# Kernel tuning notes

Measured on AMD Instinct MI355X. Metric: run time of the kernel, lower is better.

## Reference

```python
import jax, jax.numpy as jnp
import numpy as np

B, H, N, D = 2, 16, 2048, 64

def setup_inputs() -> dict:
    key = jax.random.key(0)
    ks = jax.random.split(key, 5)
    q = jax.random.normal(ks[0], (B, H, N, D), dtype=jnp.float32)
    k = jax.random.normal(ks[1], (B, H, N, D), dtype=jnp.float32)
    v = jax.random.normal(ks[2], (B, H, N, D), dtype=jnp.float32)
    # 1x1 Conv2d(heads, heads, bias=False) == HxH linear mixing over the head dim
    W_pre = jax.random.normal(ks[3], (H, H), dtype=jnp.float32) * (1.0 / jnp.sqrt(H))
    W_post = jax.random.normal(ks[4], (H, H), dtype=jnp.float32) * (1.0 / jnp.sqrt(H))
    return {"q": q, "k": k, "v": v, "W_pre": W_pre, "W_post": W_post}

def reference(q, k, v, W_pre, W_post):
    heads = q.shape[1]
    d_head = q.shape[-1]
    # original: scale = (1/sqrt(heads)) / sqrt(d_head)
    scale = 1.0 / (jnp.sqrt(jnp.float32(heads)) * jnp.sqrt(jnp.float32(d_head)))
    # pre-softmax talking heads applied to BOTH q and k (head-mixing linear)
    q = jnp.einsum('ef,bfnd->bend', W_pre, q)
    k = jnp.einsum('ef,bfnd->bend', W_pre, k)
    attn_weights = jnp.einsum('bhid,bhjd->bhij', q, k) * scale  # [B,H,N,N]
    i = q.shape[-2]
    j = k.shape[-2]
    causal_mask = jnp.triu(jnp.ones((i, j), dtype=bool), k=1)
    attn_weights = jnp.where(causal_mask, -jnp.inf, attn_weights)
    # softmax computed in float32 (dtype=torch.float32 in attn_fn)
    attn_probs = jax.nn.softmax(attn_weights.astype(jnp.float32), axis=-1)
    # dropout p=0.0 -> identity
    attn_probs = jnp.einsum('ef,bfij->beij', W_post, attn_probs)
    attn_output = jnp.einsum('bhij,bhjd->bhid', attn_probs, v)
    return attn_output
```

## Files before the change

### kernel.cpp

```cpp
#include <hip/hip_runtime.h>
#include <math.h>

typedef _Float16 Hh;
typedef __attribute__((ext_vector_type(8))) _Float16 half8;
typedef __attribute__((ext_vector_type(4))) _Float16 half4;
typedef __attribute__((ext_vector_type(4))) float float4v;

#define B_ 2
#define H_ 16
#define N_ 2048
#define D_ 64
#define ND_ (N_*D_)
#define C1 0.04508422f

#define BAR() asm volatile("s_waitcnt lgkmcnt(0)\n\ts_barrier" ::: "memory")

#define EB_JS 644
#define EB_IS 20
#define PM_ES 1280
#define PM_IS 40

__global__ __launch_bounds__(256,2) void prep_kernel(const float* __restrict__ q,
    const float* __restrict__ k, const float* __restrict__ v,
    const float* __restrict__ Wpre,
    Hh* __restrict__ qb, Hh* __restrict__ kb, Hh* __restrict__ vt2,
    float4* __restrict__ out4, float4* __restrict__ lacc4)
{
    int tid = threadIdx.x;
    int bid = blockIdx.x;
    if (bid < 512) {
        __shared__ float wsh[256];
        wsh[tid] = Wpre[tid];
        __syncthreads();
        int tensor = bid >> 8;
        int g = ((bid & 255) << 8) | tid;
        int b = g >> 15;
        int r = g & 32767;
        const float4* src = (const float4*)(tensor ? k : q);
        Hh* dst = tensor ? kb : qb;
        float4 x[16];
        #pragma unroll
        for (int f=0; f<16; f++) x[f] = src[(size_t)(b*16+f)*32768 + r];
        #pragma unroll
        for (int e=0; e<16; e++) {
            float4 a = make_float4(0.f,0.f,0.f,0.f);
            #pragma unroll
            for (int f=0; f<16; f++) {
                float wv = wsh[e*16+f];
                a.x += wv*x[f].x; a.y += wv*x[f].y; a.z += wv*x[f].z; a.w += wv*x[f].w;
            }
            half4 hv; hv[0]=(Hh)a.x; hv[1]=(Hh)a.y; hv[2]=(Hh)a.z; hv[3]=(Hh)a.w;
            *(half4*)(dst + (size_t)(b*16+e)*ND_ + (size_t)r*4) = hv;
        }
    } else if (bid < 768) {
        __shared__ Hh tile[64*48];
        int tb = bid - 512;
        int be = tb >> 3;
        int jtg = tb & 7;
        const float4* v4 = (const float4*)v;
        for (int u=0; u<8; u++) {
            int jt = jtg*8 + u;
            #pragma unroll
            for (int p=0; p<2; p++) {
                int j = p*16 + (tid>>4);
                int d4 = tid & 15;
                float4 val = v4[(size_t)be*32768 + (size_t)(jt*32+j)*16 + d4];
                tile[(d4*4+0)*48 + j] = (Hh)val.x;
                tile[(d4*4+1)*48 + j] = (Hh)val.y;
                tile[(d4*4+2)*48 + j] = (Hh)val.z;
                tile[(d4*4+3)*48 + j] = (Hh)val.w;
            }
            BAR();
            {
                int d = tid >> 2;
                int jc = (tid & 3) * 8;
                half8 o;
                #pragma unroll
                for (int z=0; z<8; z++) o[z] = tile[d*48 + jc + z];
                *(half8*)(vt2 + ((size_t)(be*64) + jt)*2048 + (size_t)tid*8) = o;
            }
            BAR();
        }
    } else {
        int zid = (bid - 768) * 256 + tid;
        float4 zz = make_float4(0.f,0.f,0.f,0.f);
        #pragma unroll
        for (int u=0; u<4; u++) out4[(size_t)u*262144 + zid] = zz;
        if (zid < 16384) lacc4[zid] = zz;
    }
}

__global__ __launch_bounds__(1024,4) void denom_kernel(const Hh* __restrict__ qb,
    const Hh* __restrict__ kb, float* __restrict__ lacc_g)
{
    int bid = blockIdx.x;
    int s = bid & 7;
    int idx = bid >> 3;
    int b = idx & 1;
    int pr = idx >> 1;
    int tid = threadIdx.x;
    int lane = tid & 63, w = tid >> 6;
    int qd = lane >> 4, c = lane & 15;

    const Hh* qh = qb + (size_t)(b*16 + w)*ND_;
    const Hh* kh = kb + (size_t)(b*16 + w)*ND_;

    for (int hf = 0; hf < 2; hf++) {
        int it = hf ? (63 - pr) : pr;
        if (s > it) continue;
        int i0 = it * 32;

        half8 aq[2][2];
        #pragma unroll
        for (int ig=0; ig<2; ig++) {
            const Hh* qr = qh + (size_t)(i0 + ig*16 + c)*64 + qd*8;
            aq[ig][0] = *(const half8*)qr;
            aq[ig][1] = *(const half8*)(qr+32);
        }
        float lacc[2][4];
        #pragma unroll
        for (int ig=0; ig<2; ig++)
            #pragma unroll
            for (int r=0; r<4; r++) lacc[ig][r] = 0.f;

        for (int jt = s; jt <= it; jt += 8) {
            int j0 = jt*32;
            #pragma unroll
            for (int jh=0; jh<2; jh++) {
                const Hh* kr = kh + (size_t)(j0 + jh*16 + c)*64 + qd*8;
                half8 b0 = *(const half8*)kr;
                half8 b1 = *(const half8*)(kr+32);
                int j = j0 + jh*16 + c;
                #pragma unroll
                for (int ig=0; ig<2; ig++) {
                    float4v sv = {0.f,0.f,0.f,0.f};
                    sv = __builtin_amdgcn_mfma_f32_16x16x32_f16(aq[ig][0], b0, sv, 0,0,0);
                    sv = __builtin_amdgcn_mfma_f32_16x16x32_f16(aq[ig][1], b1, sv, 0,0,0);
                    #pragma unroll
                    for (int r=0; r<4; r++) {
                        int i = i0 + ig*16 + qd*4 + r;
                        float ev = (j <= i) ? __builtin_amdgcn_exp2f(sv[r]*C1) : 0.f;
                        lacc[ig][r] += ev;
                    }
                }
            }
        }
        #pragma unroll
        for (int ig=0; ig<2; ig++) {
            #pragma unroll
            for (int r=0; r<4; r++) {
                float vs = lacc[ig][r];
                vs += __shfl_xor(vs, 1);
                vs += __shfl_xor(vs, 2);
                vs += __shfl_xor(vs, 4);
                vs += __shfl_xor(vs, 8);
                if (c == 0)
                    unsafeAtomicAdd(&lacc_g[(size_t)(b*16+w)*N_ + i0 + ig*16 + qd*4 + r], vs);
            }
        }
    }
}

__global__ __launch_bounds__(1024,4) void attend_kernel(const Hh* __restrict__ qb,
    const Hh* __restrict__ kb, const Hh* __restrict__ vt2,
    const float* __restrict__ lacc_g, const float* __restrict__ Wpost,
    float* __restrict__ out)
{
    __shared__ Hh Ebuf[32*EB_JS];
    __shared__ Hh Pm[16*PM_ES];

    int bid = blockIdx.x;
    int s = (bid & 7) >> 1;
    int b = bid & 1;
    int pr = bid >> 3;

    int tid = threadIdx.x;
    int lane = tid & 63, w = tid >> 6;
    int qd = lane >> 4, c = lane & 15;

    int jh2 = w & 1, ib = 4*(w >> 1);
    half4 wf;
    #pragma unroll
    for (int z=0; z<4; z++) wf[z] = (Hh)Wpost[c*16 + qd*4 + z];

    for (int hf = 0; hf < 2; hf++) {
        int it = hf ? (63 - pr) : pr;
        if (s > it) continue;
        int i0 = it * 32;

        half8 aq[2][2];
        float lgr[2][4];
        #pragma unroll
        for (int ig=0; ig<2; ig++) {
            const Hh* qr = qb + (size_t)((b*16+w)*N_ + i0 + ig*16 + c)*64 + qd*8;
            aq[ig][0] = *(const half8*)qr;
            aq[ig][1] = *(const half8*)(qr+32);
            #pragma unroll
            for (int r=0; r<4; r++)
                lgr[ig][r] = __builtin_amdgcn_logf(
                    lacc_g[(size_t)(b*16+w)*N_ + i0 + ig*16 + qd*4 + r]);
        }

        float4v acc[2][4];
        #pragma unroll
        for (int ig=0; ig<2; ig++) for (int nc=0; nc<4; nc++)
            acc[ig][nc] = (float4v){0.f,0.f,0.f,0.f};

        auto scores = [&](int jt) {
            #pragma unroll
            for (int jh=0; jh<2; jh++) {
                int jc = jt*32 + jh*16;
                const Hh* kr = kb + (size_t)((b*16+w)*N_ + jc + c)*64 + qd*8;
                half8 b0 = *(const half8*)kr;
                half8 b1 = *(const half8*)(kr+32);
                int j = jc + c;
                #pragma unroll
                for (int ig=0; ig<2; ig++) {
                    float4v sv = {0.f,0.f,0.f,0.f};
                    sv = __builtin_amdgcn_mfma_f32_16x16x32_f16(aq[ig][0], b0, sv, 0,0,0);
                    sv = __builtin_amdgcn_mfma_f32_16x16x32_f16(aq[ig][1], b1, sv, 0,0,0);
                    #pragma unroll
                    for (int r=0; r<4; r++) {
                        int i = i0 + ig*16 + qd*4 + r;
                        float ev = (j <= i) ?
                            __builtin_amdgcn_exp2f(sv[r]*C1 - lgr[ig][r]) : 0.f;
                        Ebuf[(size_t)(jh*16+c)*EB_JS + (ig*16+qd*4+r)*EB_IS + w] = (Hh)ev;
                    }
                }
            }
        };

        scores(s);
        BAR();

        for (int jt = s; jt <= it; jt += 4) {
            #pragma unroll
            for (int ii=0; ii<4; ii++) {
                int i = ib + ii;
                half4 ef = *(const half4*)&Ebuf[(jh2*16+c)*EB_JS + i*EB_IS + qd*4];
                float4v cc = {0.f,0.f,0.f,0.f};
                cc = __builtin_amdgcn_mfma_f32_16x16x16f16(ef, wf, cc, 0,0,0);
                half4 hv;
                #pragma unroll
                for (int r=0; r<4; r++) hv[r] = (Hh)cc[r];
                *(half4*)&Pm[c*PM_ES + i*PM_IS + jh2*16 + qd*4] = hv;
            }
            BAR();
            #pragma unroll
            for (int nc=0; nc<4; nc++) {
                const Hh* vr = vt2 + (size_t)((b*16+w)*64 + jt)*2048 + (nc*16+c)*32 + qd*8;
                half8 vb = *(const half8*)vr;
                #pragma unroll
                for (int ig=0; ig<2; ig++) {
                    half8 pa = *(const half8*)&Pm[w*PM_ES + (ig*16+c)*PM_IS + qd*8];
                    acc[ig][nc] = __builtin_amdgcn_mfma_f32_16x16x32_f16(pa, vb, acc[ig][nc], 0,0,0);
                }
            }
            if (jt + 4 <= it) scores(jt + 4);
            BAR();
        }

        #pragma unroll
        for (int ig=0; ig<2; ig++) {
            #pragma unroll
            for (int nc0=0; nc0<4; nc0++) {
                int nc = (nc0 + s) & 3;
                #pragma unroll
                for (int r=0; r<4; r++)
                    unsafeAtomicAdd(&out[(size_t)((b*16+w)*N_ + i0 + ig*16 + qd*4 + r)*64 + nc*16 + c],
                                    acc[ig][nc][r]);
            }
        }
    }
}

extern "C" void kernel_launch(void* const* d_in, const int* in_sizes, int n_in,
                              void* d_out, int out_size, void* d_ws, size_t ws_size,
                              hipStream_t stream) {
    const float* q     = (const float*)d_in[0];
    const float* k     = (const float*)d_in[1];
    const float* v     = (const float*)d_in[2];
    const float* Wpre  = (const float*)d_in[3];
    const float* Wpost = (const float*)d_in[4];
    float* out = (float*)d_out;

    size_t tsz = (size_t)B_*H_*N_*D_;
    Hh* qb = (Hh*)d_ws;
    Hh* kb = qb + tsz;
    Hh* vt2 = kb + tsz;
    float* lacc = (float*)(vt2 + tsz);

    prep_kernel<<<1792, 256, 0, stream>>>(q, k, v, Wpre, qb, kb, vt2,
                                          (float4*)out, (float4*)lacc);
    denom_kernel<<<512, 1024, 0, stream>>>(qb, kb, lacc);
    attend_kernel<<<256, 1024, 0, stream>>>(qb, kb, vt2, lacc, Wpost, out);
}
```

Before: 253.7 us.

## Halve attend block to 512 threads with multi-head per-wave work and K/V prefetch

The attend kernel now runs 8 waves per block instead of 16. Each wave computes scores for 4 heads over one 16-column half and accumulates PV for 2 output heads, and it writes score tiles as half4 vectors. K and V loads are issued ahead of use: the next K tile is prefetched during the W_post mixing step, and V is loaded before the barrier. The denom kernel also gets a register double-buffered K prefetch, and the Pm shared-memory padding is shrunk. The trade-off is many more live registers per wave (4 heads of Q, K and logs, plus 2x accumulators), which may lower occupancy or cause spills.

```diff
diff --git a/kernel.cpp b/kernel.cpp
--- a/kernel.cpp
+++ b/kernel.cpp
@@ -17,8 +17,8 @@
 
 #define EB_JS 644
 #define EB_IS 20
-#define PM_ES 1280
-#define PM_IS 40
+#define PM_ES 1156
+#define PM_IS 36
 
 __global__ __launch_bounds__(256,2) void prep_kernel(const float* __restrict__ q,
     const float* __restrict__ k, const float* __restrict__ v,
@@ -123,25 +123,42 @@
             #pragma unroll
             for (int r=0; r<4; r++) lacc[ig][r] = 0.f;
 
+        auto loadK = [&](int jt, half8 (&kk)[2][2]) {
+            #pragma unroll
+            for (int jh=0; jh<2; jh++) {
+                const Hh* kr = kh + (size_t)(jt*32 + jh*16 + c)*64 + qd*8;
+                kk[jh][0] = *(const half8*)kr;
+                kk[jh][1] = *(const half8*)(kr+32);
+            }
+        };
+
+        half8 ka[2][2];
+        loadK(s, ka);
         for (int jt = s; jt <= it; jt += 8) {
-            int j0 = jt*32;
+            bool more = (jt + 8 <= it);
+            half8 kn[2][2];
+            if (more) loadK(jt + 8, kn);
             #pragma unroll
             for (int jh=0; jh<2; jh++) {
-                const Hh* kr = kh + (size_t)(j0 + jh*16 + c)*64 + qd*8;
-                half8 b0 = *(const half8*)kr;
-                half8 b1 = *(const half8*)(kr+32);
-                int j = j0 + jh*16 + c;
+                int j = jt*32 + jh*16 + c;
                 #pragma unroll
                 for (int ig=0; ig<2; ig++) {
                     float4v sv = {0.f,0.f,0.f,0.f};
-                    sv = __builtin_amdgcn_mfma_f32_16x16x32_f16(aq[ig][0], b0, sv, 0,0,0);
-                    sv = __builtin_amdgcn_mfma_f32_16x16x32_f16(aq[ig][1], b1, sv, 0,0,0);
+                    sv = __builtin_amdgcn_mfma_f32_16x16x32_f16(aq[ig][0], ka[jh][0], sv, 0,0,0);
+                    sv = __builtin_amdgcn_mfma_f32_16x16x32_f16(aq[ig][1], ka[jh][1], sv, 0,0,0);
                     #pragma unroll
                     for (int r=0; r<4; r++) {
                         int i = i0 + ig*16 + qd*4 + r;
                         float ev = (j <= i) ? __builtin_amdgcn_exp2f(sv[r]*C1) : 0.f;
                         lacc[ig][r] += ev;
                     }
+                }
+            }
+            if (more) {
+                #pragma unroll
+                for (int jh=0; jh<2; jh++) {
+                    ka[jh][0] = kn[jh][0];
+                    ka[jh][1] = kn[jh][1];
                 }
             }
         }
@@ -161,7 +178,7 @@
     }
 }
 
-__global__ __launch_bounds__(1024,4) void attend_kernel(const Hh* __restrict__ qb,
+__global__ __launch_bounds__(512,2) void attend_kernel(const Hh* __restrict__ qb,
     const Hh* __restrict__ kb, const Hh* __restrict__ vt2,
     const float* __restrict__ lacc_g, const float* __restrict__ Wpost,
     float* __restrict__ out)
@@ -178,7 +195,8 @@
     int lane = tid & 63, w = tid >> 6;
     int qd = lane >> 4, c = lane & 15;
 
-    int jh2 = w & 1, ib = 4*(w >> 1);
+    int fg = w & 3, jh = w >> 2;
+    int jh2 = w & 1, ib = 8*(w >> 1);
     half4 wf;
     #pragma unroll
     for (int z=0; z<4; z++) wf[z] = (Hh)Wpost[c*16 + qd*4 + z];
@@ -188,54 +206,83 @@
         if (s > it) continue;
         int i0 = it * 32;
 
-        half8 aq[2][2];
-        float lgr[2][4];
-        #pragma unroll
-        for (int ig=0; ig<2; ig++) {
-            const Hh* qr = qb + (size_t)((b*16+w)*N_ + i0 + ig*16 + c)*64 + qd*8;
-            aq[ig][0] = *(const half8*)qr;
-            aq[ig][1] = *(const half8*)(qr+32);
-            #pragma unroll
-            for (int r=0; r<4; r++)
-                lgr[ig][r] = __builtin_amdgcn_logf(
-                    lacc_g[(size_t)(b*16+w)*N_ + i0 + ig*16 + qd*4 + r]);
-        }
-
-        float4v acc[2][4];
-        #pragma unroll
-        for (int ig=0; ig<2; ig++) for (int nc=0; nc<4; nc++)
-            acc[ig][nc] = (float4v){0.f,0.f,0.f,0.f};
-
-        auto scores = [&](int jt) {
-            #pragma unroll
-            for (int jh=0; jh<2; jh++) {
-                int jc = jt*32 + jh*16;
-                const Hh* kr = kb + (size_t)((b*16+w)*N_ + jc + c)*64 + qd*8;
-                half8 b0 = *(const half8*)kr;
-                half8 b1 = *(const half8*)(kr+32);
-                int j = jc + c;
-                #pragma unroll
-                for (int ig=0; ig<2; ig++) {
-                    float4v sv = {0.f,0.f,0.f,0.f};
-                    sv = __builtin_amdgcn_mfma_f32_16x16x32_f16(aq[ig][0], b0, sv, 0,0,0);
-                    sv = __builtin_amdgcn_mfma_f32_16x16x32_f16(aq[ig][1], b1, sv, 0,0,0);
+        half8 aq[4][2][2];
+        float lgr[4][2][4];
+        #pragma unroll
+        for (int ff=0; ff<4; ff++) {
+            int f = 4*fg + ff;
+            #pragma unroll
+            for (int ig=0; ig<2; ig++) {
+                const Hh* qr = qb + (size_t)((b*16+f)*N_ + i0 + ig*16 + c)*64 + qd*8;
+                aq[ff][ig][0] = *(const half8*)qr;
+                aq[ff][ig][1] = *(const half8*)(qr+32);
+                #pragma unroll
+                for (int r=0; r<4; r++)
+                    lgr[ff][ig][r] = __builtin_amdgcn_logf(
+                        lacc_g[(size_t)(b*16+f)*N_ + i0 + ig*16 + qd*4 + r]);
+            }
+        }
+
+        float4v acc[2][2][4];
+        #pragma unroll
+        for (int el=0; el<2; el++) for (int ig=0; ig<2; ig++) for (int nc=0; nc<4; nc++)
+            acc[el][ig][nc] = (float4v){0.f,0.f,0.f,0.f};
+
+        auto loadK = [&](int jt, half8 (&kk)[4][2]) {
+            int jc = jt*32 + jh*16;
+            #pragma unroll
+            for (int ff=0; ff<4; ff++) {
+                int f = 4*fg + ff;
+                const Hh* kr = kb + (size_t)((b*16+f)*N_ + jc + c)*64 + qd*8;
+                kk[ff][0] = *(const half8*)kr;
+                kk[ff][1] = *(const half8*)(kr+32);
+            }
+        };
+
+        auto scores = [&](int jt, half8 (&kk)[4][2]) {
+            int j = jt*32 + jh*16 + c;
+            #pragma unroll
+            for (int ig=0; ig<2; ig++) {
+                float4v sv[4];
+                #pragma unroll
+                for (int ff=0; ff<4; ff++) {
+                    float4v t = {0.f,0.f,0.f,0.f};
+                    t = __builtin_amdgcn_mfma_f32_16x16x32_f16(aq[ff][ig][0], kk[ff][0], t, 0,0,0);
+                    t = __builtin_amdgcn_mfma_f32_16x16x32_f16(aq[ff][ig][1], kk[ff][1], t, 0,0,0);
+                    sv[ff] = t;
+                }
+                #pragma unroll
+                for (int r=0; r<4; r++) {
+                    int i = i0 + ig*16 + qd*4 + r;
+                    half4 h;
                     #pragma unroll
-                    for (int r=0; r<4; r++) {
-                        int i = i0 + ig*16 + qd*4 + r;
-                        float ev = (j <= i) ?
-                            __builtin_amdgcn_exp2f(sv[r]*C1 - lgr[ig][r]) : 0.f;
-                        Ebuf[(size_t)(jh*16+c)*EB_JS + (ig*16+qd*4+r)*EB_IS + w] = (Hh)ev;
-                    }
+                    for (int ff=0; ff<4; ff++)
+                        h[ff] = (Hh)((j <= i) ?
+                            __builtin_amdgcn_exp2f(sv[ff][r]*C1 - lgr[ff][ig][r]) : 0.f);
+                    *(half4*)&Ebuf[(jh*16+c)*EB_JS + (ig*16+qd*4+r)*EB_IS + fg*4] = h;
                 }
             }
         };
 
-        scores(s);
+        half8 kk[4][2];
+        loadK(s, kk);
+        scores(s, kk);
         BAR();
 
         for (int jt = s; jt <= it; jt += 4) {
-            #pragma unroll
-            for (int ii=0; ii<4; ii++) {
+            bool more = (jt + 4 <= it);
+            half8 vv[2][4];
+            #pragma unroll
+            for (int el=0; el<2; el++) {
+                int e = 2*w + el;
+                #pragma unroll
+                for (int nc=0; nc<4; nc++)
+                    vv[el][nc] = *(const half8*)(vt2 +
+                        (size_t)((b*16+e)*64 + jt)*2048 + (nc*16+c)*32 + qd*8);
+            }
+            if (more) loadK(jt + 4, kk);
+            #pragma unroll
+            for (int ii=0; ii<8; ii++) {
                 int i = ib + ii;
                 half4 ef = *(const half4*)&Ebuf[(jh2*16+c)*EB_JS + i*EB_IS + qd*4];
                 float4v cc = {0.f,0.f,0.f,0.f};
@@ -247,28 +294,34 @@
             }
             BAR();
             #pragma unroll
-            for (int nc=0; nc<4; nc++) {
-                const Hh* vr = vt2 + (size_t)((b*16+w)*64 + jt)*2048 + (nc*16+c)*32 + qd*8;
-                half8 vb = *(const half8*)vr;
+            for (int el=0; el<2; el++) {
+                int e = 2*w + el;
                 #pragma unroll
                 for (int ig=0; ig<2; ig++) {
-                    half8 pa = *(const half8*)&Pm[w*PM_ES + (ig*16+c)*PM_IS + qd*8];
-                    acc[ig][nc] = __builtin_amdgcn_mfma_f32_16x16x32_f16(pa, vb, acc[ig][nc], 0,0,0);
-                }
-            }
-            if (jt + 4 <= it) scores(jt + 4);
+                    half8 pa = *(const half8*)&Pm[e*PM_ES + (ig*16+c)*PM_IS + qd*8];
+                    #pragma unroll
+                    for (int nc=0; nc<4; nc++)
+                        acc[el][ig][nc] = __builtin_amdgcn_mfma_f32_16x16x32_f16(
+                            pa, vv[el][nc], acc[el][ig][nc], 0,0,0);
+                }
+            }
+            if (more) scores(jt + 4, kk);
             BAR();
         }
 
         #pragma unroll
-        for (int ig=0; ig<2; ig++) {
-            #pragma unroll
-            for (int nc0=0; nc0<4; nc0++) {
-                int nc = (nc0 + s) & 3;
-                #pragma unroll
-                for (int r=0; r<4; r++)
-                    unsafeAtomicAdd(&out[(size_t)((b*16+w)*N_ + i0 + ig*16 + qd*4 + r)*64 + nc*16 + c],
-                                    acc[ig][nc][r]);
+        for (int el=0; el<2; el++) {
+            int e = 2*w + el;
+            #pragma unroll
+            for (int ig=0; ig<2; ig++) {
+                #pragma unroll
+                for (int nc0=0; nc0<4; nc0++) {
+                    int nc = (nc0 + s) & 3;
+                    #pragma unroll
+                    for (int r=0; r<4; r++)
+                        unsafeAtomicAdd(&out[(size_t)((b*16+e)*N_ + i0 + ig*16 + qd*4 + r)*64 + nc*16 + c],
+                                        acc[el][ig][nc][r]);
+                }
             }
         }
     }
@@ -293,5 +346,5 @@
     prep_kernel<<<1792, 256, 0, stream>>>(q, k, v, Wpre, qb, kb, vt2,
                                           (float4*)out, (float4*)lacc);
     denom_kernel<<<512, 1024, 0, stream>>>(qb, kb, lacc);
-    attend_kernel<<<256, 1024, 0, stream>>>(qb, kb, vt2, lacc, Wpost, out);
+    attend_kernel<<<256, 512, 0, stream>>>(qb, kb, vt2, lacc, Wpost, out);
 }
```

Result: slower. 268.9 us (+6.0%).

## Split attend key range 8 ways, prefetch K in denom, shrink Pm padding

Applied to the files above, without the earlier changes.

The attend kernel now splits each query tile's key range across 8 blocks instead of 4, doubling the grid and relying on atomic adds to combine partial outputs. Launch bounds are raised to allow more resident blocks, and the Pm shared buffer padding is reduced so two blocks can fit in LDS. The denominator kernel software-prefetches the next K tile into registers while computing the current one. This trades more atomic traffic and register pressure for more parallelism and better latency hiding.

```diff
diff --git a/kernel.cpp b/kernel.cpp
--- a/kernel.cpp
+++ b/kernel.cpp
@@ -17,8 +17,8 @@
 
 #define EB_JS 644
 #define EB_IS 20
-#define PM_ES 1280
-#define PM_IS 40
+#define PM_ES 1156
+#define PM_IS 36
 
 __global__ __launch_bounds__(256,2) void prep_kernel(const float* __restrict__ q,
     const float* __restrict__ k, const float* __restrict__ v,
@@ -123,25 +123,42 @@
             #pragma unroll
             for (int r=0; r<4; r++) lacc[ig][r] = 0.f;
 
+        auto loadK = [&](int jt, half8 (&kk)[2][2]) {
+            #pragma unroll
+            for (int jh=0; jh<2; jh++) {
+                const Hh* kr = kh + (size_t)(jt*32 + jh*16 + c)*64 + qd*8;
+                kk[jh][0] = *(const half8*)kr;
+                kk[jh][1] = *(const half8*)(kr+32);
+            }
+        };
+
+        half8 ka[2][2];
+        loadK(s, ka);
         for (int jt = s; jt <= it; jt += 8) {
-            int j0 = jt*32;
+            bool more = (jt + 8 <= it);
+            half8 kn[2][2];
+            if (more) loadK(jt + 8, kn);
             #pragma unroll
             for (int jh=0; jh<2; jh++) {
-                const Hh* kr = kh + (size_t)(j0 + jh*16 + c)*64 + qd*8;
-                half8 b0 = *(const half8*)kr;
-                half8 b1 = *(const half8*)(kr+32);
-                int j = j0 + jh*16 + c;
+                int j = jt*32 + jh*16 + c;
                 #pragma unroll
                 for (int ig=0; ig<2; ig++) {
                     float4v sv = {0.f,0.f,0.f,0.f};
-                    sv = __builtin_amdgcn_mfma_f32_16x16x32_f16(aq[ig][0], b0, sv, 0,0,0);
-                    sv = __builtin_amdgcn_mfma_f32_16x16x32_f16(aq[ig][1], b1, sv, 0,0,0);
+                    sv = __builtin_amdgcn_mfma_f32_16x16x32_f16(aq[ig][0], ka[jh][0], sv, 0,0,0);
+                    sv = __builtin_amdgcn_mfma_f32_16x16x32_f16(aq[ig][1], ka[jh][1], sv, 0,0,0);
                     #pragma unroll
                     for (int r=0; r<4; r++) {
                         int i = i0 + ig*16 + qd*4 + r;
                         float ev = (j <= i) ? __builtin_amdgcn_exp2f(sv[r]*C1) : 0.f;
                         lacc[ig][r] += ev;
                     }
+                }
+            }
+            if (more) {
+                #pragma unroll
+                for (int jh=0; jh<2; jh++) {
+                    ka[jh][0] = kn[jh][0];
+                    ka[jh][1] = kn[jh][1];
                 }
             }
         }
@@ -161,7 +178,7 @@
     }
 }
 
-__global__ __launch_bounds__(1024,4) void attend_kernel(const Hh* __restrict__ qb,
+__global__ __launch_bounds__(1024,8) void attend_kernel(const Hh* __restrict__ qb,
     const Hh* __restrict__ kb, const Hh* __restrict__ vt2,
     const float* __restrict__ lacc_g, const float* __restrict__ Wpost,
     float* __restrict__ out)
@@ -170,9 +187,10 @@
     __shared__ Hh Pm[16*PM_ES];
 
     int bid = blockIdx.x;
-    int s = (bid & 7) >> 1;
-    int b = bid & 1;
-    int pr = bid >> 3;
+    int s = bid & 7;
+    int idx = bid >> 3;
+    int b = idx & 1;
+    int pr = idx >> 1;
 
     int tid = threadIdx.x;
     int lane = tid & 63, w = tid >> 6;
@@ -233,7 +251,7 @@
         scores(s);
         BAR();
 
-        for (int jt = s; jt <= it; jt += 4) {
+        for (int jt = s; jt <= it; jt += 8) {
             #pragma unroll
             for (int ii=0; ii<4; ii++) {
                 int i = ib + ii;
@@ -256,7 +274,7 @@
                     acc[ig][nc] = __builtin_amdgcn_mfma_f32_16x16x32_f16(pa, vb, acc[ig][nc], 0,0,0);
                 }
             }
-            if (jt + 4 <= it) scores(jt + 4);
+            if (jt + 8 <= it) scores(jt + 8);
             BAR();
         }
 
@@ -293,5 +311,5 @@
     prep_kernel<<<1792, 256, 0, stream>>>(q, k, v, Wpre, qb, kb, vt2,
                                           (float4*)out, (float4*)lacc);
     denom_kernel<<<512, 1024, 0, stream>>>(qb, kb, lacc);
-    attend_kernel<<<256, 1024, 0, stream>>>(qb, kb, vt2, lacc, Wpost, out);
+    attend_kernel<<<512, 1024, 0, stream>>>(qb, kb, vt2, lacc, Wpost, out);
 }
```

Result: slower. 479.2 us (+88.9%).

## Prefetch K/V tiles in attend loop, enlarge denom row tiles, repad LDS

Applied to the files above, without the earlier changes.

The attend kernel now loads the next K and V tiles into registers before the current tile's P·W_post and P·V work, so global-load latency overlaps with MFMA compute. The denom kernel handles 64 query rows per block, half as many blocks, which reuses each K fragment across four row groups. The Pm LDS strides are re-padded, and the launch-bounds hint is dropped from prep_kernel. The prefetch buffers raise register pressure, which could lower occupancy, and the denom blocks now do more work each.

```diff
diff --git a/kernel.cpp b/kernel.cpp
--- a/kernel.cpp
+++ b/kernel.cpp
@@ -17,10 +17,10 @@
 
 #define EB_JS 644
 #define EB_IS 20
-#define PM_ES 1280
-#define PM_IS 40
-
-__global__ __launch_bounds__(256,2) void prep_kernel(const float* __restrict__ q,
+#define PM_ES 1156
+#define PM_IS 36
+
+__global__ void prep_kernel(const float* __restrict__ q,
     const float* __restrict__ k, const float* __restrict__ v,
     const float* __restrict__ Wpre,
     Hh* __restrict__ qb, Hh* __restrict__ kb, Hh* __restrict__ vt2,
@@ -106,24 +106,24 @@
     const Hh* kh = kb + (size_t)(b*16 + w)*ND_;
 
     for (int hf = 0; hf < 2; hf++) {
-        int it = hf ? (63 - pr) : pr;
-        if (s > it) continue;
-        int i0 = it * 32;
-
-        half8 aq[2][2];
-        #pragma unroll
-        for (int ig=0; ig<2; ig++) {
+        int it = hf ? (31 - pr) : pr;
+        int i0 = it * 64;
+
+        half8 aq[4][2];
+        #pragma unroll
+        for (int ig=0; ig<4; ig++) {
             const Hh* qr = qh + (size_t)(i0 + ig*16 + c)*64 + qd*8;
             aq[ig][0] = *(const half8*)qr;
             aq[ig][1] = *(const half8*)(qr+32);
         }
-        float lacc[2][4];
-        #pragma unroll
-        for (int ig=0; ig<2; ig++)
+        float lacc[4][4];
+        #pragma unroll
+        for (int ig=0; ig<4; ig++)
             #pragma unroll
             for (int r=0; r<4; r++) lacc[ig][r] = 0.f;
 
-        for (int jt = s; jt <= it; jt += 8) {
+        int jtmax = 2*it + 1;
+        for (int jt = s; jt <= jtmax; jt += 8) {
             int j0 = jt*32;
             #pragma unroll
             for (int jh=0; jh<2; jh++) {
@@ -132,7 +132,7 @@
                 half8 b1 = *(const half8*)(kr+32);
                 int j = j0 + jh*16 + c;
                 #pragma unroll
-                for (int ig=0; ig<2; ig++) {
+                for (int ig=0; ig<4; ig++) {
                     float4v sv = {0.f,0.f,0.f,0.f};
                     sv = __builtin_amdgcn_mfma_f32_16x16x32_f16(aq[ig][0], b0, sv, 0,0,0);
                     sv = __builtin_amdgcn_mfma_f32_16x16x32_f16(aq[ig][1], b1, sv, 0,0,0);
@@ -146,7 +146,7 @@
             }
         }
         #pragma unroll
-        for (int ig=0; ig<2; ig++) {
+        for (int ig=0; ig<4; ig++) {
             #pragma unroll
             for (int r=0; r<4; r++) {
                 float vs = lacc[ig][r];
@@ -206,19 +206,30 @@
         for (int ig=0; ig<2; ig++) for (int nc=0; nc<4; nc++)
             acc[ig][nc] = (float4v){0.f,0.f,0.f,0.f};
 
-        auto scores = [&](int jt) {
+        auto loadK = [&](int jt, half8 (&kk)[2][2]) {
             #pragma unroll
             for (int jh=0; jh<2; jh++) {
-                int jc = jt*32 + jh*16;
-                const Hh* kr = kb + (size_t)((b*16+w)*N_ + jc + c)*64 + qd*8;
-                half8 b0 = *(const half8*)kr;
-                half8 b1 = *(const half8*)(kr+32);
-                int j = jc + c;
+                const Hh* kr = kb + (size_t)((b*16+w)*N_ + jt*32 + jh*16 + c)*64 + qd*8;
+                kk[jh][0] = *(const half8*)kr;
+                kk[jh][1] = *(const half8*)(kr+32);
+            }
+        };
+        auto loadV = [&](int jt, half8 (&vv)[4]) {
+            #pragma unroll
+            for (int nc=0; nc<4; nc++)
+                vv[nc] = *(const half8*)(vt2 +
+                    (size_t)((b*16+w)*64 + jt)*2048 + (nc*16+c)*32 + qd*8);
+        };
+
+        auto scores = [&](int jt, half8 (&kk)[2][2]) {
+            #pragma unroll
+            for (int jh=0; jh<2; jh++) {
+                int j = jt*32 + jh*16 + c;
                 #pragma unroll
                 for (int ig=0; ig<2; ig++) {
                     float4v sv = {0.f,0.f,0.f,0.f};
-                    sv = __builtin_amdgcn_mfma_f32_16x16x32_f16(aq[ig][0], b0, sv, 0,0,0);
-                    sv = __builtin_amdgcn_mfma_f32_16x16x32_f16(aq[ig][1], b1, sv, 0,0,0);
+                    sv = __builtin_amdgcn_mfma_f32_16x16x32_f16(aq[ig][0], kk[jh][0], sv, 0,0,0);
+                    sv = __builtin_amdgcn_mfma_f32_16x16x32_f16(aq[ig][1], kk[jh][1], sv, 0,0,0);
                     #pragma unroll
                     for (int r=0; r<4; r++) {
                         int i = i0 + ig*16 + qd*4 + r;
@@ -230,10 +241,16 @@
             }
         };
 
-        scores(s);
+        half8 kk[2][2], vv[4];
+        loadK(s, kk);
+        loadV(s, vv);
+        scores(s, kk);
         BAR();
 
         for (int jt = s; jt <= it; jt += 4) {
+            bool more = (jt + 4 <= it);
+            half8 kn[2][2], vn[4];
+            if (more) { loadK(jt + 4, kn); loadV(jt + 4, vn); }
             #pragma unroll
             for (int ii=0; ii<4; ii++) {
                 int i = ib + ii;
@@ -248,15 +265,17 @@
             BAR();
             #pragma unroll
             for (int nc=0; nc<4; nc++) {
-                const Hh* vr = vt2 + (size_t)((b*16+w)*64 + jt)*2048 + (nc*16+c)*32 + qd*8;
-                half8 vb = *(const half8*)vr;
                 #pragma unroll
                 for (int ig=0; ig<2; ig++) {
                     half8 pa = *(const half8*)&Pm[w*PM_ES + (ig*16+c)*PM_IS + qd*8];
-                    acc[ig][nc] = __builtin_amdgcn_mfma_f32_16x16x32_f16(pa, vb, acc[ig][nc], 0,0,0);
+                    acc[ig][nc] = __builtin_amdgcn_mfma_f32_16x16x32_f16(pa, vv[nc], acc[ig][nc], 0,0,0);
                 }
             }
-            if (jt + 4 <= it) scores(jt + 4);
+            if (more) {
+                scores(jt + 4, kn);
+                #pragma unroll
+                for (int nc=0; nc<4; nc++) vv[nc] = vn[nc];
+            }
             BAR();
         }
 
@@ -292,6 +311,6 @@
 
     prep_kernel<<<1792, 256, 0, stream>>>(q, k, v, Wpre, qb, kb, vt2,
                                           (float4*)out, (float4*)lacc);
-    denom_kernel<<<512, 1024, 0, stream>>>(qb, kb, lacc);
+    denom_kernel<<<256, 1024, 0, stream>>>(qb, kb, lacc);
     attend_kernel<<<256, 1024, 0, stream>>>(qb, kb, vt2, lacc, Wpost, out);
 }
```

Measured after the change: 235.1 us. -7.3%, faster.
